# Kernel tuning notes

Hardware: AMD Instinct MI355X
Metric: run time of the kernel (lower is better)

Reference implementation:

```python
import jax, jax.numpy as jnp
import numpy as np

BINWIDTHS = (5000, 1000, 500, 200, 100, 50, 25)
WINDOW = (0, 200000)
TOTAL = WINDOW[1] - WINDOW[0]

def _level_shapes():
    shapes = []
    cw = TOTAL
    for bw in BINWIDTHS:
        nb = cw // bw
        ns = TOTAL // (bw * nb)
        shapes.append((ns, nb))
        cw = bw
    return shapes

LEVEL_SHAPES = _level_shapes()          # [(1,40),(40,5),(200,2),(500,2),(1000,2),(2000,2),(4000,2)]
NBINS = [ns * nb for ns, nb in LEVEL_SHAPES]
N_FINAL = TOTAL // BINWIDTHS[-1]        # 8000

N_REGIONS = 500
N_CLUSTERS = 20
N_REGIONS_OI = 256
N_CELLS = 10000
N_CUTS = 500000
DELTA_P_SCALE = 1.5


def setup_inputs() -> dict:
    key = jax.random.key(0)
    ks = jax.random.split(key, 32)
    inp = {}
    inp["components"] = jax.random.normal(ks[0], (N_CLUSTERS, N_CLUSTERS), jnp.float32)
    for lvl, (ns, nb) in enumerate(LEVEL_SHAPES):
        inp[f"w_bias_{lvl}"] = jax.random.normal(ks[1 + lvl], (N_REGIONS, ns, nb), jnp.float32) * 0.05
        inp[f"w_delta_{lvl}"] = jax.random.normal(ks[10 + lvl], (N_REGIONS, N_CLUSTERS, ns * nb), jnp.float32) * 0.02
    inp["regions_oi"] = jax.random.randint(ks[20], (N_REGIONS_OI,), 0, N_REGIONS)
    inp["local_region_ix"] = jax.random.randint(ks[21], (N_CUTS,), 0, N_REGIONS_OI)
    inp["local_cell_ix"] = jax.random.randint(ks[22], (N_CUTS,), 0, N_CELLS)
    inp["clustering_indices"] = jax.random.randint(ks[23], (N_CELLS,), 0, N_CLUSTERS)
    inp["coordinates"] = jax.random.randint(ks[24], (N_CUTS,), WINDOW[0], WINDOW[1])
    return inp


def _calculate_w(components, w_biases, w_deltas, regions_oi):
    R = regions_oi.shape[0]
    C = components.shape[1]
    scale = jnp.float32(DELTA_P_SCALE)
    log_scale = jnp.log(scale)
    half_log_2pi = jnp.float32(0.5 * np.log(2.0 * np.pi))
    w = jnp.zeros((R, C, N_FINAL), jnp.float32)
    kl = jnp.float32(0.0)
    for lvl, (ns, nb) in enumerate(LEVEL_SHAPES):
        wb = w_biases[lvl][regions_oi]                    # (R, ns, nb) irregular gather
        Wd = w_deltas[lvl][regions_oi]                    # (R, C, ns*nb) irregular gather
        # MultiLinear: einsum('ab,cad->cbd', components, W)
        wd = jnp.einsum('ab,cad->cbd', components, Wd)    # (R, C, ns*nb)
        wd = wd.reshape(R, C, ns, nb)
        w_level = (wb[:, None, :, :] + wd).reshape(R, C, NBINS[lvl])
        rep = N_FINAL // NBINS[lvl]
        w = (w.reshape(R, C, NBINS[lvl], rep) + w_level[..., None]).reshape(R, C, N_FINAL)
        # Normal(0, scale).log_prob(wd), summed
        kl = kl + jnp.sum(-0.5 * (wd / scale) ** 2 - log_scale - half_log_2pi)
    w = jax.nn.log_softmax(w, axis=-1) - jnp.log(jnp.float32(BINWIDTHS[-1]))
    return w, kl


def reference(components, w_bias_0, w_bias_1, w_bias_2, w_bias_3, w_bias_4, w_bias_5, w_bias_6,
              w_delta_0, w_delta_1, w_delta_2, w_delta_3, w_delta_4, w_delta_5, w_delta_6,
              regions_oi, local_region_ix, local_cell_ix, clustering_indices, coordinates):
    w_biases = [w_bias_0, w_bias_1, w_bias_2, w_bias_3, w_bias_4, w_bias_5, w_bias_6]
    w_deltas = [w_delta_0, w_delta_1, w_delta_2, w_delta_3, w_delta_4, w_delta_5, w_delta_6]
    w, kl = _calculate_w(components, w_biases, w_deltas, regions_oi)
    coords = jnp.clip(coordinates, WINDOW[0], WINDOW[1] - 1) - WINDOW[0]
    bin_ix = coords // BINWIDTHS[-1]
    cluster_ix = clustering_indices[local_cell_ix]
    likelihood = w[local_region_ix, cluster_ix, bin_ix]   # (N_CUTS,)
    return likelihood, kl
```

## Files before the change

### kernel.cpp

```cpp
#include <hip/hip_runtime.h>
#include <hip/hip_bf16.h>
#include <math.h>


#define NROI 256
#define NC 20
#define NFINAL 8000
#define NCUTS 500000
#define TB 256
#define NTILE 32
#define UTSTR 40
#define NKL (NROI * NTILE + NROI)

typedef __attribute__((ext_vector_type(8))) short bf16x8;
typedef __attribute__((ext_vector_type(4))) float f32x4;

static __device__ __forceinline__ ushort bfr(float x) {
    union { __hip_bfloat16 h; ushort u; } v;
    v.h = __float2bfloat16(x);
    return v.u;
}
static __device__ __forceinline__ bf16x8 pack8(float4 a, float4 b) {
    union { bf16x8 v; ushort s[8]; } u;
    u.s[0] = bfr(a.x); u.s[1] = bfr(a.y); u.s[2] = bfr(a.z); u.s[3] = bfr(a.w);
    u.s[4] = bfr(b.x); u.s[5] = bfr(b.y); u.s[6] = bfr(b.z); u.s[7] = bfr(b.w);
    return u.v;
}

__global__ void k_init(const float* __restrict__ comp,
                       float* __restrict__ g2, float* __restrict__ gfull,
                       ushort* __restrict__ compPad)
{
    const int tid = threadIdx.x;
    for (int i = tid; i < 400; i += 256) {
        const int a = i / 20, b = i % 20;
        float s = 0.f;
#pragma unroll
        for (int c = 0; c < 20; c++) s += comp[a * 20 + c] * comp[b * 20 + c];
        g2[i] = (b < a) ? 0.f : (b == a ? s : 2.f * s);
    }
    for (int i = tid; i < 1024; i += 256) {
        const int rr = i >> 5, cc = i & 31;
        float s = 0.f;
        if (rr < 20 && cc < 20) {
#pragma unroll
            for (int c = 0; c < 20; c++) s += comp[rr * 20 + c] * comp[cc * 20 + c];
        }
        gfull[i] = s;
        const float v = (rr < 20 && cc < 20) ? comp[cc * 20 + rr] : 0.f;
        compPad[i] = bfr(v);
    }
}

__global__ __launch_bounds__(256, 2) void k_main(
    const float* __restrict__ gfull, const ushort* __restrict__ compPad,
    const float* __restrict__ wb0, const float* __restrict__ wd0,
    const float* __restrict__ wb1, const float* __restrict__ wd1,
    const float* __restrict__ wb2, const float* __restrict__ wd2,
    const float* __restrict__ wb3, const float* __restrict__ wd3,
    const float* __restrict__ wb4, const float* __restrict__ wd4,
    const float* __restrict__ wb5, const float* __restrict__ wd5,
    const float* __restrict__ wb6, const float* __restrict__ wd6,
    const int* __restrict__ regions_oi,
    __hip_bfloat16* __restrict__ w2,
    float* __restrict__ s_part, float* __restrict__ klbuf)
{
    __shared__ ushort Utsh[TB * UTSTR];
    __shared__ float cs_sh[20 * 64];
    __shared__ float biasf[TB];
    __shared__ float sexp_sh[20];
    __shared__ float klp[4];

    const int tid = threadIdx.x;
    const int wv = tid >> 6, ln = tid & 63;
    const int l15 = ln & 15, lg = ln >> 4;
    const int r = blockIdx.x >> 5;
    const int tile = blockIdx.x & 31;
    const int base = tile << 8;
    const int r0 = regions_oi[r];

    const float* __restrict__ p6 = wd6 + (size_t)r0 * (20 * 8000);
    const float* __restrict__ p5 = wd5 + (size_t)r0 * (20 * 4000);
    const float* __restrict__ p4 = wd4 + (size_t)r0 * (20 * 2000);
    const float* __restrict__ p3 = wd3 + (size_t)r0 * (20 * 1000);
    const float* __restrict__ p2 = wd2 + (size_t)r0 * (20 * 400);
    const float* __restrict__ p1 = wd1 + (size_t)r0 * (20 * 200);
    const float* __restrict__ p0 = wd0 + (size_t)r0 * (20 * 40);
    const float* __restrict__ b6 = wb6 + (size_t)r0 * 8000;
    const float* __restrict__ b5 = wb5 + (size_t)r0 * 4000;
    const float* __restrict__ b4 = wb4 + (size_t)r0 * 2000;
    const float* __restrict__ b3 = wb3 + (size_t)r0 * 1000;
    const float* __restrict__ b2 = wb2 + (size_t)r0 * 400;
    const float* __restrict__ b1 = wb1 + (size_t)r0 * 200;
    const float* __restrict__ b0 = wb0 + (size_t)r0 * 40;

    if (tid < 20) sexp_sh[tid] = 0.f;

    {
        f32x4 s00 = {0.f, 0.f, 0.f, 0.f};
        f32x4 s10 = {0.f, 0.f, 0.f, 0.f};
        f32x4 s11 = {0.f, 0.f, 0.f, 0.f};
#pragma unroll
        for (int i = 0; i < 4; i++) {
            const int ch = wv + 4 * i;
            if (ch < 15) {
                const float* P; int K, col0;
                if (ch < 8)       { P = p6; K = 8000; col0 = base + ch * 32; }
                else if (ch < 12) { P = p5; K = 4000; col0 = (base >> 1) + (ch - 8) * 32; }
                else if (ch < 14) { P = p4; K = 2000; col0 = (base >> 2) + (ch - 12) * 32; }
                else              { P = p3; K = 1000; col0 = (base >> 3); }
                const int cb = col0 + lg * 8;
                bf16x8 flo = {0,0,0,0,0,0,0,0}, fhi = {0,0,0,0,0,0,0,0};
                if (cb < K) {
                    const float4 xa = *(const float4*)(P + (size_t)l15 * K + cb);
                    const float4 xb = *(const float4*)(P + (size_t)l15 * K + cb + 4);
                    flo = pack8(xa, xb);
                    if (l15 < 4) {
                        const float4 ya = *(const float4*)(P + (size_t)(16 + l15) * K + cb);
                        const float4 yb = *(const float4*)(P + (size_t)(16 + l15) * K + cb + 4);
                        fhi = pack8(ya, yb);
                    }
                }
                s00 = __builtin_amdgcn_mfma_f32_16x16x32_bf16(flo, flo, s00, 0, 0, 0);
                s10 = __builtin_amdgcn_mfma_f32_16x16x32_bf16(fhi, flo, s10, 0, 0, 0);
                s11 = __builtin_amdgcn_mfma_f32_16x16x32_bf16(fhi, fhi, s11, 0, 0, 0);
            }
        }
        float qp = 0.f;
#pragma unroll
        for (int reg = 0; reg < 4; reg++) {
            const int rlo = lg * 4 + reg, rhi = 16 + lg * 4 + reg;
            qp += gfull[rlo * 32 + l15] * s00[reg];
            qp += 2.f * gfull[rhi * 32 + l15] * s10[reg];
            qp += gfull[rhi * 32 + 16 + l15] * s11[reg];
        }
#pragma unroll
        for (int off = 32; off > 0; off >>= 1) qp += __shfl_down(qp, off, 64);
        if (ln == 0) klp[wv] = qp;
    }

#pragma unroll
    for (int it = 0; it < 5; it++) {
        const int u = it * 256 + tid;
        const int a = u >> 6, qd = u & 63;
        const int j = base + 4 * qd;
        float v = 0.f;
        if (j < NFINAL)
            v = p4[a * 2000 + (j >> 2)] + p3[a * 1000 + (j >> 3)]
              + p2[a * 400 + j / 20] + p1[a * 200 + j / 40]
              + p0[a * 40 + j / 200];
        cs_sh[a * 64 + qd] = v;
    }
    {
        const int j = base + tid;
        float v = 0.f;
        if (j < NFINAL)
            v = b6[j] + b5[j >> 1] + b4[j >> 2] + b3[j >> 3]
              + b2[j / 20] + b1[j / 40] + b0[j / 200];
        biasf[tid] = v;
    }
    __syncthreads();

    {
        const int j = base + tid;
        const bool ok = j < NFINAL;
        const int qd = tid >> 2;
#pragma unroll
        for (int it = 0; it < 5; it++) {
            float u[4];
#pragma unroll
            for (int i = 0; i < 4; i++) {
                const int a = 4 * it + i;
                float x6 = 0.f, x5 = 0.f;
                if (ok) {
                    x6 = p6[(size_t)a * 8000 + j];
                    x5 = p5[a * 4000 + (j >> 1)];
                }
                u[i] = x6 + x5 + cs_sh[a * 64 + qd];
            }
            *(ushort4*)&Utsh[tid * UTSTR + 4 * it] =
                make_ushort4(bfr(u[0]), bfr(u[1]), bfr(u[2]), bfr(u[3]));
        }
        const ushort4 z4 = make_ushort4(0, 0, 0, 0);
        *(ushort4*)&Utsh[tid * UTSTR + 20] = z4;
        *(ushort4*)&Utsh[tid * UTSTR + 24] = z4;
        *(ushort4*)&Utsh[tid * UTSTR + 28] = z4;
    }
    __syncthreads();

    {
        bf16x8 fA0 = *(const bf16x8*)&compPad[l15 * 32 + lg * 8];
        bf16x8 fA1 = *(const bf16x8*)&compPad[(16 + l15) * 32 + lg * 8];
        float sA[4] = {0.f, 0.f, 0.f, 0.f};
        float sB[4] = {0.f, 0.f, 0.f, 0.f};
#pragma unroll
        for (int t = 0; t < 4; t++) {
            const int nt = 4 * t + wv;
            bf16x8 fB = *(const bf16x8*)&Utsh[(nt * 16 + l15) * UTSTR + lg * 8];
            const f32x4 z = {0.f, 0.f, 0.f, 0.f};
            f32x4 c0 = __builtin_amdgcn_mfma_f32_16x16x32_bf16(fA0, fB, z, 0, 0, 0);
            f32x4 c1 = __builtin_amdgcn_mfma_f32_16x16x32_bf16(fA1, fB, z, 0, 0, 0);
            const int binl = nt * 16 + l15;
            const int bin = base + binl;
            const float bi = biasf[binl];
            if (bin < NFINAL) {
#pragma unroll
                for (int reg = 0; reg < 4; reg++) {
                    const int c = lg * 4 + reg;
                    const float w = bi + c0[reg];
                    w2[(size_t)(r * 20 + c) * 8000 + bin] = __float2bfloat16(w);
                    sA[reg] += __expf(w);
                }
                if (lg == 0) {
#pragma unroll
                    for (int reg = 0; reg < 4; reg++) {
                        const float w = bi + c1[reg];
                        w2[(size_t)(r * 20 + 16 + reg) * 8000 + bin] = __float2bfloat16(w);
                        sB[reg] += __expf(w);
                    }
                }
            }
        }
#pragma unroll
        for (int reg = 0; reg < 4; reg++) {
            float s = sA[reg];
            s += __shfl_xor(s, 1, 64); s += __shfl_xor(s, 2, 64);
            s += __shfl_xor(s, 4, 64); s += __shfl_xor(s, 8, 64);
            if (l15 == 0) atomicAdd(&sexp_sh[lg * 4 + reg], s);
            float sb = sB[reg];
            sb += __shfl_xor(sb, 1, 64); sb += __shfl_xor(sb, 2, 64);
            sb += __shfl_xor(sb, 4, 64); sb += __shfl_xor(sb, 8, 64);
            if (ln == 0) atomicAdd(&sexp_sh[16 + reg], sb);
        }
    }
    __syncthreads();
    if (tid < 20) s_part[((size_t)r * NTILE + tile) * 20 + tid] = sexp_sh[tid];
    if (tid == 0) klbuf[blockIdx.x] = klp[0] + klp[1] + klp[2] + klp[3];
}

__global__ __launch_bounds__(256, 2) void k_klc(
    const float* __restrict__ g2,
    const float* __restrict__ wd0, const float* __restrict__ wd1,
    const float* __restrict__ wd2,
    const int* __restrict__ regions_oi, float* __restrict__ klbuf)
{
    __shared__ float klp[4];
    const int tid = threadIdx.x;
    const int r0 = regions_oi[blockIdx.x];
    const float* __restrict__ p2 = wd2 + (size_t)r0 * (20 * 400);
    const float* __restrict__ p1 = wd1 + (size_t)r0 * (20 * 200);
    const float* __restrict__ p0 = wd0 + (size_t)r0 * (20 * 40);

    float q = 0.f;
#pragma unroll 1
    for (int it = 0; it < 3; it++) {
        const int u = it * 256 + tid;
        if (u >= 640) break;
        const float* P; int K, col;
        if (u < 400)      { P = p2; K = 400; col = u; }
        else if (u < 600) { P = p1; K = 200; col = u - 400; }
        else              { P = p0; K = 40;  col = u - 600; }
        float x[20];
#pragma unroll
        for (int a = 0; a < 20; a++) x[a] = P[a * K + col];
#pragma unroll
        for (int a = 0; a < 20; a++) {
            float t = g2[a * 21] * x[a];
#pragma unroll
            for (int b = a + 1; b < 20; b++) t += g2[a * 20 + b] * x[b];
            q += x[a] * t;
        }
    }
#pragma unroll
    for (int off = 32; off > 0; off >>= 1) q += __shfl_down(q, off, 64);
    if ((tid & 63) == 0) klp[tid >> 6] = q;
    __syncthreads();
    if (tid == 0)
        klbuf[NROI * NTILE + blockIdx.x] = klp[0] + klp[1] + klp[2] + klp[3];
}

__global__ void k_klred(const float* __restrict__ klbuf, float* __restrict__ kl)
{
    __shared__ float part[4];
    const int tid = threadIdx.x;
    float s = 0.f;
    for (int i = tid; i < NKL; i += 256) s += klbuf[i];
#pragma unroll
    for (int off = 32; off > 0; off >>= 1) s += __shfl_down(s, off, 64);
    if ((tid & 63) == 0) part[tid >> 6] = s;
    __syncthreads();
    if (tid == 0)
        kl[0] = (float)(-80076800.0 * 1.3244036413128371)
              + (part[0] + part[1] + part[2] + part[3]) * (-0.5f / 2.25f);
}

__global__ void k_sub(const float* __restrict__ s_part, float* __restrict__ sub)
{
    const int i = blockIdx.x * 256 + threadIdx.x;
    if (i >= NROI * NC) return;
    const int r = i / 20, c = i % 20;
    float s = 0.f;
#pragma unroll 1
    for (int t = 0; t < NTILE; t++) s += s_part[(size_t)(r * NTILE + t) * 20 + c];
    sub[i] = logf(s) + 3.2188758248682006f;
}

__global__ void k_gather(const int* __restrict__ lri, const int* __restrict__ lci,
                         const int* __restrict__ cli, const int* __restrict__ coords,
                         const __hip_bfloat16* __restrict__ w2,
                         const float* __restrict__ sub,
                         float* __restrict__ out)
{
    const int i = blockIdx.x * 256 + threadIdx.x;
    if (i >= NCUTS) return;
    const int r = lri[i];
    const int c = cli[lci[i]];
    int co = coords[i];
    co = co < 0 ? 0 : (co > 199999 ? 199999 : co);
    const int bin = co / 25;
    const int rc = r * 20 + c;
    out[i] = __bfloat162float(w2[(size_t)rc * 8000 + bin]) - sub[rc];
}

extern "C" void kernel_launch(void* const* d_in, const int* in_sizes, int n_in,
                              void* d_out, int out_size, void* d_ws, size_t ws_size,
                              hipStream_t stream)
{
    const float* comp = (const float*)d_in[0];
    const float* wb[7];
    const float* wd[7];
    if (in_sizes[2] == 400000) {
        for (int l = 0; l < 7; l++) { wb[l] = (const float*)d_in[1 + 2 * l]; wd[l] = (const float*)d_in[2 + 2 * l]; }
    } else {
        for (int l = 0; l < 7; l++) { wb[l] = (const float*)d_in[1 + l]; wd[l] = (const float*)d_in[8 + l]; }
    }
    const int* regions_oi = (const int*)d_in[15];
    const int* lri   = (const int*)d_in[16];
    const int* lci   = (const int*)d_in[17];
    const int* cli   = (const int*)d_in[18];
    const int* coords= (const int*)d_in[19];
    float* out = (float*)d_out;

    __hip_bfloat16* w2 = (__hip_bfloat16*)d_ws;
    float* s_part = (float*)(w2 + (size_t)NROI * NC * NFINAL);
    float* sub    = s_part + (size_t)NROI * NTILE * 20;
    float* g2buf  = sub + NROI * NC;
    float* gfull  = g2buf + 400;
    ushort* compPad = (ushort*)(gfull + 1024);
    float* klbuf  = (float*)(compPad + 1024);
    const size_t need = (size_t)NROI * NC * NFINAL * 2
                      + ((size_t)NROI * NTILE * 20 + NROI * NC + 400 + 1024 + 512
                         + NKL) * sizeof(float);
    if (ws_size < need) return;

    k_init<<<1, 256, 0, stream>>>(comp, g2buf, gfull, compPad);
    k_main<<<NROI * NTILE, 256, 0, stream>>>(gfull, compPad,
        wb[0], wd[0], wb[1], wd[1], wb[2], wd[2], wb[3], wd[3],
        wb[4], wd[4], wb[5], wd[5], wb[6], wd[6],
        regions_oi, w2, s_part, klbuf);
    k_klc<<<NROI, 256, 0, stream>>>(g2buf, wd[0], wd[1], wd[2],
        regions_oi, klbuf);
    k_klred<<<1, 256, 0, stream>>>(klbuf, out + NCUTS);
    k_sub<<<(NROI * NC + 255) / 256, 256, 0, stream>>>(s_part, sub);
    k_gather<<<(NCUTS + 255) / 256, 256, 0, stream>>>(lri, lci, cli, coords,
        w2, sub, out);
}
```

Baseline: 202.9 us.

## Split main kernel and recompute gathered likelihood from staged pre-projection rows

The fused main kernel is split into a staging kernel and a separate sum-exp kernel. The staging kernel writes the per-bin pre-projection delta vectors (bf16, 20 per bin) and the summed biases to global memory. The sum-exp kernel reloads them to do the MFMA projection and exp sums. The gather kernel no longer reads a materialised full w tensor: it rebuilds each needed value as bias plus a 20-term dot with the transposed components. This removes the large bf16 w write but adds an extra global round trip of the staged buffer, another launch, and more arithmetic per gathered cut.

Result: slower. 225.0 us (+10.9%).

```diff
diff --git a/kernel.cpp b/kernel.cpp
--- a/kernel.cpp
+++ b/kernel.cpp
@@ -9,7 +9,6 @@
 #define NCUTS 500000
 #define TB 256
 #define NTILE 32
-#define UTSTR 40
 #define NKL (NROI * NTILE + NROI)
 
 typedef __attribute__((ext_vector_type(8))) short bf16x8;
@@ -19,6 +18,11 @@
     union { __hip_bfloat16 h; ushort u; } v;
     v.h = __float2bfloat16(x);
     return v.u;
+}
+static __device__ __forceinline__ float b2f(ushort u) {
+    union { float f; unsigned x; } v;
+    v.x = ((unsigned)u) << 16;
+    return v.f;
 }
 static __device__ __forceinline__ bf16x8 pack8(float4 a, float4 b) {
     union { bf16x8 v; ushort s[8]; } u;
@@ -29,7 +33,7 @@
 
 __global__ void k_init(const float* __restrict__ comp,
                        float* __restrict__ g2, float* __restrict__ gfull,
-                       ushort* __restrict__ compPad)
+                       float* __restrict__ compT, ushort* __restrict__ compPad)
 {
     const int tid = threadIdx.x;
     for (int i = tid; i < 400; i += 256) {
@@ -38,6 +42,7 @@
 #pragma unroll
         for (int c = 0; c < 20; c++) s += comp[a * 20 + c] * comp[b * 20 + c];
         g2[i] = (b < a) ? 0.f : (b == a ? s : 2.f * s);
+        compT[i] = comp[b * 20 + a];
     }
     for (int i = tid; i < 1024; i += 256) {
         const int rr = i >> 5, cc = i & 31;
@@ -52,8 +57,8 @@
     }
 }
 
-__global__ __launch_bounds__(256, 2) void k_main(
-    const float* __restrict__ gfull, const ushort* __restrict__ compPad,
+__global__ __launch_bounds__(256, 2) void k_stage(
+    const float* __restrict__ gfull,
     const float* __restrict__ wb0, const float* __restrict__ wd0,
     const float* __restrict__ wb1, const float* __restrict__ wd1,
     const float* __restrict__ wb2, const float* __restrict__ wd2,
@@ -62,13 +67,10 @@
     const float* __restrict__ wb5, const float* __restrict__ wd5,
     const float* __restrict__ wb6, const float* __restrict__ wd6,
     const int* __restrict__ regions_oi,
-    __hip_bfloat16* __restrict__ w2,
-    float* __restrict__ s_part, float* __restrict__ klbuf)
-{
-    __shared__ ushort Utsh[TB * UTSTR];
+    ushort* __restrict__ Ubuf, float* __restrict__ biasG,
+    float* __restrict__ klbuf)
+{
     __shared__ float cs_sh[20 * 64];
-    __shared__ float biasf[TB];
-    __shared__ float sexp_sh[20];
     __shared__ float klp[4];
 
     const int tid = threadIdx.x;
@@ -94,7 +96,50 @@
     const float* __restrict__ b1 = wb1 + (size_t)r0 * 200;
     const float* __restrict__ b0 = wb0 + (size_t)r0 * 40;
 
-    if (tid < 20) sexp_sh[tid] = 0.f;
+#pragma unroll
+    for (int it = 0; it < 5; it++) {
+        const int u = it * 256 + tid;
+        const int a = u >> 6, qd = u & 63;
+        const int j = base + 4 * qd;
+        float v = 0.f;
+        if (j < NFINAL)
+            v = p4[a * 2000 + (j >> 2)] + p3[a * 1000 + (j >> 3)]
+              + p2[a * 400 + j / 20] + p1[a * 200 + j / 40]
+              + p0[a * 40 + j / 200];
+        cs_sh[a * 64 + qd] = v;
+    }
+    {
+        const int j = base + tid;
+        if (j < NFINAL)
+            biasG[(size_t)r * 8000 + j] =
+                b6[j] + b5[j >> 1] + b4[j >> 2] + b3[j >> 3]
+              + b2[j / 20] + b1[j / 40] + b0[j / 200];
+    }
+    __syncthreads();
+
+    {
+        const int j = base + tid;
+        const bool ok = j < NFINAL;
+        const int qd = tid >> 2;
+        ushort* urow = Ubuf + (size_t)(r * 8000 + (ok ? j : 0)) * 20;
+#pragma unroll
+        for (int it = 0; it < 5; it++) {
+            float u[4];
+#pragma unroll
+            for (int i = 0; i < 4; i++) {
+                const int a = 4 * it + i;
+                float x6 = 0.f, x5 = 0.f;
+                if (ok) {
+                    x6 = p6[(size_t)a * 8000 + j];
+                    x5 = p5[a * 4000 + (j >> 1)];
+                }
+                u[i] = x6 + x5 + cs_sh[a * 64 + qd];
+            }
+            if (ok)
+                *(ushort4*)(urow + 4 * it) =
+                    make_ushort4(bfr(u[0]), bfr(u[1]), bfr(u[2]), bfr(u[3]));
+        }
+    }
 
     {
         f32x4 s00 = {0.f, 0.f, 0.f, 0.f};
@@ -138,104 +183,72 @@
         for (int off = 32; off > 0; off >>= 1) qp += __shfl_down(qp, off, 64);
         if (ln == 0) klp[wv] = qp;
     }
-
-#pragma unroll
-    for (int it = 0; it < 5; it++) {
-        const int u = it * 256 + tid;
-        const int a = u >> 6, qd = u & 63;
-        const int j = base + 4 * qd;
-        float v = 0.f;
-        if (j < NFINAL)
-            v = p4[a * 2000 + (j >> 2)] + p3[a * 1000 + (j >> 3)]
-              + p2[a * 400 + j / 20] + p1[a * 200 + j / 40]
-              + p0[a * 40 + j / 200];
-        cs_sh[a * 64 + qd] = v;
-    }
-    {
-        const int j = base + tid;
-        float v = 0.f;
-        if (j < NFINAL)
-            v = b6[j] + b5[j >> 1] + b4[j >> 2] + b3[j >> 3]
-              + b2[j / 20] + b1[j / 40] + b0[j / 200];
-        biasf[tid] = v;
-    }
     __syncthreads();
-
-    {
-        const int j = base + tid;
-        const bool ok = j < NFINAL;
-        const int qd = tid >> 2;
-#pragma unroll
-        for (int it = 0; it < 5; it++) {
-            float u[4];
-#pragma unroll
-            for (int i = 0; i < 4; i++) {
-                const int a = 4 * it + i;
-                float x6 = 0.f, x5 = 0.f;
-                if (ok) {
-                    x6 = p6[(size_t)a * 8000 + j];
-                    x5 = p5[a * 4000 + (j >> 1)];
-                }
-                u[i] = x6 + x5 + cs_sh[a * 64 + qd];
+    if (tid == 0) klbuf[blockIdx.x] = klp[0] + klp[1] + klp[2] + klp[3];
+}
+
+__global__ __launch_bounds__(256, 2) void k_sexp(
+    const ushort* __restrict__ compPad,
+    const ushort* __restrict__ Ubuf, const float* __restrict__ biasG,
+    float* __restrict__ s_part)
+{
+    const int tid = threadIdx.x;
+    const int wv = tid >> 6, ln = tid & 63;
+    const int l15 = ln & 15, lg = ln >> 4;
+    const int r = blockIdx.x >> 5;
+    const int tile = blockIdx.x & 31;
+    const int base = tile << 8;
+
+    bf16x8 fA0 = *(const bf16x8*)&compPad[l15 * 32 + lg * 8];
+    bf16x8 fA1 = *(const bf16x8*)&compPad[(16 + l15) * 32 + lg * 8];
+
+    float sA[4] = {0.f, 0.f, 0.f, 0.f};
+    float sB[4] = {0.f, 0.f, 0.f, 0.f};
+#pragma unroll
+    for (int t = 0; t < 4; t++) {
+        const int nt = 4 * t + wv;
+        const int bin = base + nt * 16 + l15;
+        const bool ok = bin < NFINAL;
+        bf16x8 fb = {0, 0, 0, 0, 0, 0, 0, 0};
+        float bi = 0.f;
+        if (ok) {
+            const ushort* row = Ubuf + (size_t)(r * 8000 + bin) * 20;
+            union { bf16x8 v; ushort4 q[2]; } u;
+            u.q[0] = make_ushort4(0, 0, 0, 0);
+            u.q[1] = make_ushort4(0, 0, 0, 0);
+            if (lg < 2) {
+                u.q[0] = *(const ushort4*)(row + lg * 8);
+                u.q[1] = *(const ushort4*)(row + lg * 8 + 4);
+            } else if (lg == 2) {
+                u.q[0] = *(const ushort4*)(row + 16);
             }
-            *(ushort4*)&Utsh[tid * UTSTR + 4 * it] =
-                make_ushort4(bfr(u[0]), bfr(u[1]), bfr(u[2]), bfr(u[3]));
-        }
-        const ushort4 z4 = make_ushort4(0, 0, 0, 0);
-        *(ushort4*)&Utsh[tid * UTSTR + 20] = z4;
-        *(ushort4*)&Utsh[tid * UTSTR + 24] = z4;
-        *(ushort4*)&Utsh[tid * UTSTR + 28] = z4;
-    }
-    __syncthreads();
-
-    {
-        bf16x8 fA0 = *(const bf16x8*)&compPad[l15 * 32 + lg * 8];
-        bf16x8 fA1 = *(const bf16x8*)&compPad[(16 + l15) * 32 + lg * 8];
-        float sA[4] = {0.f, 0.f, 0.f, 0.f};
-        float sB[4] = {0.f, 0.f, 0.f, 0.f};
-#pragma unroll
-        for (int t = 0; t < 4; t++) {
-            const int nt = 4 * t + wv;
-            bf16x8 fB = *(const bf16x8*)&Utsh[(nt * 16 + l15) * UTSTR + lg * 8];
-            const f32x4 z = {0.f, 0.f, 0.f, 0.f};
-            f32x4 c0 = __builtin_amdgcn_mfma_f32_16x16x32_bf16(fA0, fB, z, 0, 0, 0);
-            f32x4 c1 = __builtin_amdgcn_mfma_f32_16x16x32_bf16(fA1, fB, z, 0, 0, 0);
-            const int binl = nt * 16 + l15;
-            const int bin = base + binl;
-            const float bi = biasf[binl];
-            if (bin < NFINAL) {
-#pragma unroll
-                for (int reg = 0; reg < 4; reg++) {
-                    const int c = lg * 4 + reg;
-                    const float w = bi + c0[reg];
-                    w2[(size_t)(r * 20 + c) * 8000 + bin] = __float2bfloat16(w);
-                    sA[reg] += __expf(w);
-                }
-                if (lg == 0) {
-#pragma unroll
-                    for (int reg = 0; reg < 4; reg++) {
-                        const float w = bi + c1[reg];
-                        w2[(size_t)(r * 20 + 16 + reg) * 8000 + bin] = __float2bfloat16(w);
-                        sB[reg] += __expf(w);
-                    }
-                }
+            fb = u.v;
+            bi = biasG[(size_t)r * 8000 + bin];
+        }
+        const f32x4 z = {0.f, 0.f, 0.f, 0.f};
+        f32x4 c0 = __builtin_amdgcn_mfma_f32_16x16x32_bf16(fA0, fb, z, 0, 0, 0);
+        f32x4 c1 = __builtin_amdgcn_mfma_f32_16x16x32_bf16(fA1, fb, z, 0, 0, 0);
+        if (ok) {
+#pragma unroll
+            for (int reg = 0; reg < 4; reg++) {
+                sA[reg] += __expf(bi + c0[reg]);
+                if (lg == 0) sB[reg] += __expf(bi + c1[reg]);
             }
         }
-#pragma unroll
-        for (int reg = 0; reg < 4; reg++) {
-            float s = sA[reg];
-            s += __shfl_xor(s, 1, 64); s += __shfl_xor(s, 2, 64);
-            s += __shfl_xor(s, 4, 64); s += __shfl_xor(s, 8, 64);
-            if (l15 == 0) atomicAdd(&sexp_sh[lg * 4 + reg], s);
-            float sb = sB[reg];
-            sb += __shfl_xor(sb, 1, 64); sb += __shfl_xor(sb, 2, 64);
-            sb += __shfl_xor(sb, 4, 64); sb += __shfl_xor(sb, 8, 64);
-            if (ln == 0) atomicAdd(&sexp_sh[16 + reg], sb);
-        }
-    }
-    __syncthreads();
-    if (tid < 20) s_part[((size_t)r * NTILE + tile) * 20 + tid] = sexp_sh[tid];
-    if (tid == 0) klbuf[blockIdx.x] = klp[0] + klp[1] + klp[2] + klp[3];
+    }
+    float* spp = s_part + ((size_t)blockIdx.x * 4 + wv) * 20;
+#pragma unroll
+    for (int reg = 0; reg < 4; reg++) {
+        float s = sA[reg];
+        s += __shfl_xor(s, 1, 64); s += __shfl_xor(s, 2, 64);
+        s += __shfl_xor(s, 4, 64); s += __shfl_xor(s, 8, 64);
+        if (l15 == 0) spp[lg * 4 + reg] = s;
+        float sb = sB[reg];
+        sb += __shfl_xor(sb, 1, 64); sb += __shfl_xor(sb, 2, 64);
+        sb += __shfl_xor(sb, 4, 64); sb += __shfl_xor(sb, 8, 64);
+        sb += __shfl_xor(sb, 16, 64); sb += __shfl_xor(sb, 32, 64);
+        if (ln == 0) spp[16 + reg] = sb;
+    }
 }
 
 __global__ __launch_bounds__(256, 2) void k_klc(
@@ -264,11 +277,11 @@
 #pragma unroll
         for (int a = 0; a < 20; a++) x[a] = P[a * K + col];
 #pragma unroll
-        for (int a = 0; a < 20; a++) {
-            float t = g2[a * 21] * x[a];
-#pragma unroll
-            for (int b = a + 1; b < 20; b++) t += g2[a * 20 + b] * x[b];
-            q += x[a] * t;
+        for (int a_ = 0; a_ < 20; a_++) {
+            float t_ = g2[a_ * 21] * x[a_];
+#pragma unroll
+            for (int b_ = a_ + 1; b_ < 20; b_++) t_ += g2[a_ * 20 + b_] * x[b_];
+            q += x[a_] * t_;
         }
     }
 #pragma unroll
@@ -301,13 +314,16 @@
     const int r = i / 20, c = i % 20;
     float s = 0.f;
 #pragma unroll 1
-    for (int t = 0; t < NTILE; t++) s += s_part[(size_t)(r * NTILE + t) * 20 + c];
+    for (int t = 0; t < NTILE * 4; t++)
+        s += s_part[((size_t)r * NTILE * 4 + t) * 20 + c];
     sub[i] = logf(s) + 3.2188758248682006f;
 }
 
 __global__ void k_gather(const int* __restrict__ lri, const int* __restrict__ lci,
                          const int* __restrict__ cli, const int* __restrict__ coords,
-                         const __hip_bfloat16* __restrict__ w2,
+                         const ushort* __restrict__ Ubuf,
+                         const float* __restrict__ biasG,
+                         const float* __restrict__ compT,
                          const float* __restrict__ sub,
                          float* __restrict__ out)
 {
@@ -318,8 +334,16 @@
     int co = coords[i];
     co = co < 0 ? 0 : (co > 199999 ? 199999 : co);
     const int bin = co / 25;
-    const int rc = r * 20 + c;
-    out[i] = __bfloat162float(w2[(size_t)rc * 8000 + bin]) - sub[rc];
+    const ushort* row = Ubuf + (size_t)(r * 8000 + bin) * 20;
+    const float* cc = compT + c * 20;
+    float w = biasG[(size_t)r * 8000 + bin];
+#pragma unroll
+    for (int k = 0; k < 5; k++) {
+        const ushort4 u4 = *(const ushort4*)(row + 4 * k);
+        w += cc[4 * k + 0] * b2f(u4.x) + cc[4 * k + 1] * b2f(u4.y)
+           + cc[4 * k + 2] * b2f(u4.z) + cc[4 * k + 3] * b2f(u4.w);
+    }
+    out[i] = w - sub[r * 20 + c];
 }
 
 extern "C" void kernel_launch(void* const* d_in, const int* in_sizes, int n_in,
@@ -341,27 +365,31 @@
     const int* coords= (const int*)d_in[19];
     float* out = (float*)d_out;
 
-    __hip_bfloat16* w2 = (__hip_bfloat16*)d_ws;
-    float* s_part = (float*)(w2 + (size_t)NROI * NC * NFINAL);
-    float* sub    = s_part + (size_t)NROI * NTILE * 20;
+    ushort* Ubuf  = (ushort*)d_ws;
+    float* biasG  = (float*)(Ubuf + (size_t)NROI * NFINAL * 20);
+    float* s_part = biasG + (size_t)NROI * NFINAL;
+    float* sub    = s_part + (size_t)NROI * NTILE * 4 * 20;
     float* g2buf  = sub + NROI * NC;
     float* gfull  = g2buf + 400;
-    ushort* compPad = (ushort*)(gfull + 1024);
+    float* compT  = gfull + 1024;
+    ushort* compPad = (ushort*)(compT + 400);
     float* klbuf  = (float*)(compPad + 1024);
-    const size_t need = (size_t)NROI * NC * NFINAL * 2
-                      + ((size_t)NROI * NTILE * 20 + NROI * NC + 400 + 1024 + 512
-                         + NKL) * sizeof(float);
+    const size_t need = (size_t)NROI * NFINAL * 20 * 2
+                      + ((size_t)NROI * NFINAL + NROI * NTILE * 4 * 20
+                         + NROI * NC + 400 + 1024 + 400 + 512 + NKL)
+                        * sizeof(float);
     if (ws_size < need) return;
 
-    k_init<<<1, 256, 0, stream>>>(comp, g2buf, gfull, compPad);
-    k_main<<<NROI * NTILE, 256, 0, stream>>>(gfull, compPad,
+    k_init<<<1, 256, 0, stream>>>(comp, g2buf, gfull, compT, compPad);
+    k_stage<<<NROI * NTILE, 256, 0, stream>>>(gfull,
         wb[0], wd[0], wb[1], wd[1], wb[2], wd[2], wb[3], wd[3],
         wb[4], wd[4], wb[5], wd[5], wb[6], wd[6],
-        regions_oi, w2, s_part, klbuf);
+        regions_oi, Ubuf, biasG, klbuf);
+    k_sexp<<<NROI * NTILE, 256, 0, stream>>>(compPad, Ubuf, biasG, s_part);
     k_klc<<<NROI, 256, 0, stream>>>(g2buf, wd[0], wd[1], wd[2],
         regions_oi, klbuf);
     k_klred<<<1, 256, 0, stream>>>(klbuf, out + NCUTS);
     k_sub<<<(NROI * NC + 255) / 256, 256, 0, stream>>>(s_part, sub);
     k_gather<<<(NCUTS + 255) / 256, 256, 0, stream>>>(lri, lci, cli, coords,
-        w2, sub, out);
-}
+        Ubuf, biasG, compT, sub, out);
+}
```
